# Performance work log

Hardware: AMD Instinct MI355X
Metric: run time of the kernel (lower is better)

The kernel has to match this reference:

```python
import jax, jax.numpy as jnp
import numpy as np

B, C_IN, C_OUT, N, K = 16, 128, 128, 4096, 16


def setup_inputs() -> dict:
    key = jax.random.key(0)
    k1, k2, k3, k4 = jax.random.split(key, 4)
    x = jax.random.normal(k1, (B, C_IN, N, 1), dtype=jnp.float32)
    edge_index = jax.random.randint(k2, (2, B, N, K), 0, N, dtype=jnp.int32)
    # 1x1 conv weight of BasicConv([C_IN, C_OUT], 'relu', None, bias=False)
    W = jax.random.normal(k3, (C_OUT, C_IN), dtype=jnp.float32) * (1.0 / np.sqrt(C_IN))
    # module bias param, initialized to zeros; use random here to exercise the add
    bias = jax.random.normal(k4, (1, C_OUT, 1, 1), dtype=jnp.float32) * 0.01
    return {"x": x, "edge_index": edge_index, "W": W, "bias": bias}


def reference(x, edge_index, W, bias):
    b, _, n, _ = x.shape
    # BasicConv: 1x1 conv (no bias) + ReLU
    h = jax.nn.relu(jnp.einsum('oi,binu->bonu', W, x))  # [B, C_out, N, 1]
    h2 = h[..., 0]                                       # [B, C_out, N]
    # add_self_loops: append self index along neighbor dim
    self_idx = jnp.broadcast_to(jnp.arange(n, dtype=edge_index.dtype)[None, None, :, None],
                                (2, b, n, 1))
    ei = jnp.concatenate([edge_index, self_idx], axis=-1)  # [2, B, N, K+1]
    idx = ei[0]                                            # [B, N, K+1]
    deg = ei.shape[-1]
    norm = 1.0 / deg
    # batched_index_select: gather neighbor features -> [B, C_out, N, K+1]
    x_j = jax.vmap(lambda hb, ib: hb[:, ib])(h2, idx)
    aggr = (x_j * norm).sum(axis=-1, keepdims=True)        # [B, C_out, N, 1]
    return aggr + bias
```

## Files before the change

### kernel.cpp

```cpp
#include <hip/hip_runtime.h>

#define B_    16
#define CIN_  128
#define COUT_ 128
#define N_    4096
#define K_    16

typedef __attribute__((ext_vector_type(8))) short bf16x8;
typedef __attribute__((ext_vector_type(4))) float f32x4;
typedef __attribute__((ext_vector_type(4))) int   i32x4;

__device__ inline unsigned short f2bf(float f) {
  unsigned u = __float_as_uint(f);
  u += 0x7fffu + ((u >> 16) & 1u);
  return (unsigned short)(u >> 16);
}

__global__ __launch_bounds__(256) void convW_k(
    const float* __restrict__ W, unsigned short* __restrict__ Wbf) {
  int id = blockIdx.x * 256 + threadIdx.x;
  float4 v = reinterpret_cast<const float4*>(W)[id];
  unsigned p0 = (unsigned)f2bf(v.x) | ((unsigned)f2bf(v.y) << 16);
  unsigned p1 = (unsigned)f2bf(v.z) | ((unsigned)f2bf(v.w) << 16);
  *reinterpret_cast<uint2*>(Wbf + 4 * id) = make_uint2(p0, p1);
}

__global__ __launch_bounds__(1024, 4) void gemm_relu_k(
    const unsigned short* __restrict__ Wbf, const float* __restrict__ x,
    unsigned short* __restrict__ h) {
  __shared__ unsigned short Wl[128 * 136];
  __shared__ unsigned short He[256 * 144];
  const int tid  = threadIdx.x;
  const int l    = blockIdx.x;
  const int slot = l >> 3;
  const int b    = ((l & 7) << 1) | (slot >> 4);
  const int n0   = (slot & 15) * 256;

#pragma unroll
  for (int r = 0; r < 2; ++r) {
    int id  = tid + 1024 * r;
    int co  = id >> 4;
    int seg = id & 15;
    uint4 v = reinterpret_cast<const uint4*>(Wbf)[id];
    *reinterpret_cast<uint4*>(&Wl[co * 136 + 8 * seg]) = v;
  }
  __syncthreads();

  const int lane = tid & 63;
  const int w    = tid >> 6;
  const int m    = lane & 15;
  const int quad = lane >> 4;

  const float* xb = x + (size_t)b * CIN_ * N_ + n0 + 16 * w + m;
  bf16x8 a[4];
#pragma unroll
  for (int s = 0; s < 4; ++s)
#pragma unroll
    for (int j = 0; j < 8; ++j)
      a[s][j] = (short)f2bf(xb[(size_t)(32 * s + 8 * quad + j) * N_]);

  const int nrow = 16 * w + 4 * quad;
#pragma unroll
  for (int t = 0; t < 8; ++t) {
    f32x4 c = {0.f, 0.f, 0.f, 0.f};
#pragma unroll
    for (int s = 0; s < 4; ++s) {
      bf16x8 bf = *reinterpret_cast<const bf16x8*>(
          &Wl[(16 * t + m) * 136 + 32 * s + 8 * quad]);
      c = __builtin_amdgcn_mfma_f32_16x16x32_bf16(a[s], bf, c, 0, 0, 0);
    }
    int co = 16 * t + m;
#pragma unroll
    for (int r = 0; r < 4; ++r) {
      float v = c[r] > 0.f ? c[r] : 0.f;
      He[(nrow + r) * 144 + co] = f2bf(v);
    }
  }
  __syncthreads();

  unsigned short* hb = h + ((size_t)b * N_ + n0) * COUT_;
  const int seg = tid & 15;
  const int nr  = tid >> 4;
#pragma unroll
  for (int p = 0; p < 4; ++p) {
    int n = nr + 64 * p;
    uint4 v = *reinterpret_cast<const uint4*>(&He[n * 144 + 8 * seg]);
    *reinterpret_cast<uint4*>(hb + (size_t)n * COUT_ + 8 * seg) = v;
  }
}

__global__ __launch_bounds__(256, 4) void aggr_k(
    const unsigned short* __restrict__ h, const int* __restrict__ ei,
    const float* __restrict__ bias, float* __restrict__ out) {
  __shared__ int idx_t[17 * 64];
  const int tid  = threadIdx.x;
  const int l    = blockIdx.x;
  const int rest = l >> 3;
  const int b    = ((l & 7) << 1) | (rest >> 6);
  const int n0   = (rest & 63) * 64;

  {
    int n  = tid >> 2;
    int kq = tid & 3;
    i32x4 v = __builtin_nontemporal_load(
        reinterpret_cast<const i32x4*>(ei + ((size_t)b * N_ + n0 + n) * K_) + kq);
    idx_t[(4 * kq + 0) * 64 + n] = v.x;
    idx_t[(4 * kq + 1) * 64 + n] = v.y;
    idx_t[(4 * kq + 2) * 64 + n] = v.z;
    idx_t[(4 * kq + 3) * 64 + n] = v.w;
    if (tid < 64) idx_t[16 * 64 + tid] = n0 + tid;
  }
  __syncthreads();

  const int q = tid & 15;
  const int g = tid >> 4;
  const unsigned short* hb = h + (size_t)b * N_ * COUT_;

  float acc[4][8];
#pragma unroll
  for (int j = 0; j < 4; ++j)
#pragma unroll
    for (int c = 0; c < 8; ++c) acc[j][c] = 0.f;

#pragma unroll 2
  for (int k = 0; k < 17; ++k) {
    uint4 v[4];
#pragma unroll
    for (int j = 0; j < 4; ++j) {
      int node = idx_t[k * 64 + 4 * g + j];
      v[j] = *reinterpret_cast<const uint4*>(hb + (size_t)node * COUT_ + 8 * q);
    }
#pragma unroll
    for (int j = 0; j < 4; ++j) {
      acc[j][0] += __uint_as_float(v[j].x << 16);
      acc[j][1] += __uint_as_float(v[j].x & 0xffff0000u);
      acc[j][2] += __uint_as_float(v[j].y << 16);
      acc[j][3] += __uint_as_float(v[j].y & 0xffff0000u);
      acc[j][4] += __uint_as_float(v[j].z << 16);
      acc[j][5] += __uint_as_float(v[j].z & 0xffff0000u);
      acc[j][6] += __uint_as_float(v[j].w << 16);
      acc[j][7] += __uint_as_float(v[j].w & 0xffff0000u);
    }
  }

  const float norm = 1.0f / 17.0f;
  const float4 bv0 = *reinterpret_cast<const float4*>(bias + 8 * q);
  const float4 bv1 = *reinterpret_cast<const float4*>(bias + 8 * q + 4);
  float* ob = out + (size_t)b * COUT_ * N_ + n0 + 4 * g;
#pragma unroll
  for (int c = 0; c < 8; ++c) {
    int co = 8 * q + c;
    float bb = (c < 4) ? ((c == 0) ? bv0.x : (c == 1) ? bv0.y : (c == 2) ? bv0.z : bv0.w)
                       : ((c == 4) ? bv1.x : (c == 5) ? bv1.y : (c == 6) ? bv1.z : bv1.w);
    float4 r;
    r.x = acc[0][c] * norm + bb;
    r.y = acc[1][c] * norm + bb;
    r.z = acc[2][c] * norm + bb;
    r.w = acc[3][c] * norm + bb;
    *reinterpret_cast<float4*>(ob + (size_t)co * N_) = r;
  }
}

extern "C" void kernel_launch(void* const* d_in, const int* in_sizes, int n_in,
                              void* d_out, int out_size, void* d_ws, size_t ws_size,
                              hipStream_t stream) {
  const float* x    = (const float*)d_in[0];
  const int*   ei   = (const int*)d_in[1];
  const float* W    = (const float*)d_in[2];
  const float* bias = (const float*)d_in[3];
  float* out = (float*)d_out;
  unsigned short* h   = (unsigned short*)d_ws;
  unsigned short* Wbf = (unsigned short*)((char*)d_ws + (size_t)B_ * N_ * COUT_ * 2);

  convW_k<<<dim3(16), 256, 0, stream>>>(W, Wbf);
  gemm_relu_k<<<dim3(256), 1024, 0, stream>>>(Wbf, x, h);
  aggr_k<<<dim3(B_ * N_ / 64), 256, 0, stream>>>(h, ei, bias, out);
}
```

Before: 112.7 us.

## Fuse weight conversion, GEMM and aggregation into one kernel with per-batch-group barrier

Merges the three launches into one persistent-style kernel. Each block converts W to bf16 itself and issues the x loads before the W staging. After writing its h tile it waits on a global atomic barrier shared by the 32 blocks that cover the same pair of batches, then performs the neighbor aggregation for four 64-node tiles, reusing the He shared buffer for the index tables. This removes launch gaps and the separate W conversion pass. In exchange it relies on all 32 blocks of a group being co-resident, adds a spin-wait, and converts W redundantly in every block.

```diff
diff --git a/kernel.cpp b/kernel.cpp
--- a/kernel.cpp
+++ b/kernel.cpp
@@ -16,35 +16,19 @@
   return (unsigned short)(u >> 16);
 }
 
-__global__ __launch_bounds__(256) void convW_k(
-    const float* __restrict__ W, unsigned short* __restrict__ Wbf) {
-  int id = blockIdx.x * 256 + threadIdx.x;
-  float4 v = reinterpret_cast<const float4*>(W)[id];
-  unsigned p0 = (unsigned)f2bf(v.x) | ((unsigned)f2bf(v.y) << 16);
-  unsigned p1 = (unsigned)f2bf(v.z) | ((unsigned)f2bf(v.w) << 16);
-  *reinterpret_cast<uint2*>(Wbf + 4 * id) = make_uint2(p0, p1);
-}
+__device__ int g_bar[8 * 32];
 
-__global__ __launch_bounds__(1024, 4) void gemm_relu_k(
-    const unsigned short* __restrict__ Wbf, const float* __restrict__ x,
-    unsigned short* __restrict__ h) {
+__global__ __launch_bounds__(1024, 4) void fused_k(
+    const float* __restrict__ W, const float* __restrict__ x,
+    const int* __restrict__ ei, const float* __restrict__ bias,
+    float* __restrict__ out, unsigned short* __restrict__ h) {
   __shared__ unsigned short Wl[128 * 136];
-  __shared__ unsigned short He[256 * 144];
+  __shared__ __align__(16) unsigned short He[256 * 144];
   const int tid  = threadIdx.x;
   const int l    = blockIdx.x;
   const int slot = l >> 3;
   const int b    = ((l & 7) << 1) | (slot >> 4);
   const int n0   = (slot & 15) * 256;
-
-#pragma unroll
-  for (int r = 0; r < 2; ++r) {
-    int id  = tid + 1024 * r;
-    int co  = id >> 4;
-    int seg = id & 15;
-    uint4 v = reinterpret_cast<const uint4*>(Wbf)[id];
-    *reinterpret_cast<uint4*>(&Wl[co * 136 + 8 * seg]) = v;
-  }
-  __syncthreads();
 
   const int lane = tid & 63;
   const int w    = tid >> 6;
@@ -52,12 +36,36 @@
   const int quad = lane >> 4;
 
   const float* xb = x + (size_t)b * CIN_ * N_ + n0 + 16 * w + m;
+  float xa[32];
+#pragma unroll
+  for (int s = 0; s < 4; ++s)
+#pragma unroll
+    for (int j = 0; j < 8; ++j)
+      xa[8 * s + j] = xb[(size_t)(32 * s + 8 * quad + j) * N_];
+
+#pragma unroll
+  for (int r = 0; r < 2; ++r) {
+    int id  = tid + 1024 * r;
+    int co  = id >> 4;
+    int seg = id & 15;
+    const float4* wp = reinterpret_cast<const float4*>(W + co * CIN_ + 8 * seg);
+    float4 v0 = wp[0];
+    float4 v1 = wp[1];
+    unsigned p0 = (unsigned)f2bf(v0.x) | ((unsigned)f2bf(v0.y) << 16);
+    unsigned p1 = (unsigned)f2bf(v0.z) | ((unsigned)f2bf(v0.w) << 16);
+    unsigned p2 = (unsigned)f2bf(v1.x) | ((unsigned)f2bf(v1.y) << 16);
+    unsigned p3 = (unsigned)f2bf(v1.z) | ((unsigned)f2bf(v1.w) << 16);
+    *reinterpret_cast<uint4*>(&Wl[co * 136 + 8 * seg]) =
+        make_uint4(p0, p1, p2, p3);
+  }
+  __syncthreads();
+
   bf16x8 a[4];
 #pragma unroll
   for (int s = 0; s < 4; ++s)
 #pragma unroll
     for (int j = 0; j < 8; ++j)
-      a[s][j] = (short)f2bf(xb[(size_t)(32 * s + 8 * quad + j) * N_]);
+      a[s][j] = (short)f2bf(xa[8 * s + j]);
 
   const int nrow = 16 * w + 4 * quad;
 #pragma unroll
@@ -78,43 +86,53 @@
   }
   __syncthreads();
 
-  unsigned short* hb = h + ((size_t)b * N_ + n0) * COUT_;
-  const int seg = tid & 15;
-  const int nr  = tid >> 4;
+  {
+    unsigned short* hb = h + ((size_t)b * N_ + n0) * COUT_;
+    const int seg = tid & 15;
+    const int nr  = tid >> 4;
 #pragma unroll
-  for (int p = 0; p < 4; ++p) {
-    int n = nr + 64 * p;
-    uint4 v = *reinterpret_cast<const uint4*>(&He[n * 144 + 8 * seg]);
-    *reinterpret_cast<uint4*>(hb + (size_t)n * COUT_ + 8 * seg) = v;
+    for (int p = 0; p < 4; ++p) {
+      int n = nr + 64 * p;
+      uint4 v = *reinterpret_cast<const uint4*>(&He[n * 144 + 8 * seg]);
+      *reinterpret_cast<uint4*>(hb + (size_t)n * COUT_ + 8 * seg) = v;
+    }
   }
-}
 
-__global__ __launch_bounds__(256, 4) void aggr_k(
-    const unsigned short* __restrict__ h, const int* __restrict__ ei,
-    const float* __restrict__ bias, float* __restrict__ out) {
-  __shared__ int idx_t[17 * 64];
-  const int tid  = threadIdx.x;
-  const int l    = blockIdx.x;
-  const int rest = l >> 3;
-  const int b    = ((l & 7) << 1) | (rest >> 6);
-  const int n0   = (rest & 63) * 64;
-
-  {
-    int n  = tid >> 2;
-    int kq = tid & 3;
-    i32x4 v = __builtin_nontemporal_load(
-        reinterpret_cast<const i32x4*>(ei + ((size_t)b * N_ + n0 + n) * K_) + kq);
-    idx_t[(4 * kq + 0) * 64 + n] = v.x;
-    idx_t[(4 * kq + 1) * 64 + n] = v.y;
-    idx_t[(4 * kq + 2) * 64 + n] = v.z;
-    idx_t[(4 * kq + 3) * 64 + n] = v.w;
-    if (tid < 64) idx_t[16 * 64 + tid] = n0 + tid;
+  __syncthreads();
+  if (tid == 0) {
+    int* cnt = &g_bar[(l & 7) * 32];
+    int base = __hip_atomic_fetch_add(cnt, 1, __ATOMIC_RELEASE,
+                                      __HIP_MEMORY_SCOPE_AGENT);
+    int target = (base & ~31) + 32;
+    while (__hip_atomic_load(cnt, __ATOMIC_RELAXED,
+                             __HIP_MEMORY_SCOPE_AGENT) < target)
+      __builtin_amdgcn_s_sleep(4);
   }
   __syncthreads();
 
-  const int q = tid & 15;
-  const int g = tid >> 4;
-  const unsigned short* hb = h + (size_t)b * N_ * COUT_;
+  const int s4    = tid >> 8;
+  const int t2    = tid & 255;
+  const int rest2 = (l >> 3) + 32 * s4;
+  const int b2    = ((l & 7) << 1) | (rest2 >> 6);
+  const int n02   = (rest2 & 63) * 64;
+  int* idxs = reinterpret_cast<int*>(He) + s4 * (17 * 64);
+
+  {
+    int n  = t2 >> 2;
+    int kq = t2 & 3;
+    i32x4 v = __builtin_nontemporal_load(
+        reinterpret_cast<const i32x4*>(ei + ((size_t)b2 * N_ + n02 + n) * K_) + kq);
+    idxs[(4 * kq + 0) * 64 + n] = v.x;
+    idxs[(4 * kq + 1) * 64 + n] = v.y;
+    idxs[(4 * kq + 2) * 64 + n] = v.z;
+    idxs[(4 * kq + 3) * 64 + n] = v.w;
+    if (t2 < 64) idxs[16 * 64 + t2] = n02 + t2;
+  }
+  __syncthreads();
+
+  const int q = t2 & 15;
+  const int g = t2 >> 4;
+  const unsigned short* hb2 = h + (size_t)b2 * N_ * COUT_;
 
   float acc[4][8];
 #pragma unroll
@@ -127,8 +145,8 @@
     uint4 v[4];
 #pragma unroll
     for (int j = 0; j < 4; ++j) {
-      int node = idx_t[k * 64 + 4 * g + j];
-      v[j] = *reinterpret_cast<const uint4*>(hb + (size_t)node * COUT_ + 8 * q);
+      int node = idxs[k * 64 + 4 * g + j];
+      v[j] = *reinterpret_cast<const uint4*>(hb2 + (size_t)node * COUT_ + 8 * q);
     }
 #pragma unroll
     for (int j = 0; j < 4; ++j) {
@@ -146,7 +164,7 @@
   const float norm = 1.0f / 17.0f;
   const float4 bv0 = *reinterpret_cast<const float4*>(bias + 8 * q);
   const float4 bv1 = *reinterpret_cast<const float4*>(bias + 8 * q + 4);
-  float* ob = out + (size_t)b * COUT_ * N_ + n0 + 4 * g;
+  float* ob = out + (size_t)b2 * COUT_ * N_ + n02 + 4 * g;
 #pragma unroll
   for (int c = 0; c < 8; ++c) {
     int co = 8 * q + c;
@@ -169,10 +187,7 @@
   const float* W    = (const float*)d_in[2];
   const float* bias = (const float*)d_in[3];
   float* out = (float*)d_out;
-  unsigned short* h   = (unsigned short*)d_ws;
-  unsigned short* Wbf = (unsigned short*)((char*)d_ws + (size_t)B_ * N_ * COUT_ * 2);
+  unsigned short* h = (unsigned short*)d_ws;
 
-  convW_k<<<dim3(16), 256, 0, stream>>>(W, Wbf);
-  gemm_relu_k<<<dim3(256), 1024, 0, stream>>>(Wbf, x, h);
-  aggr_k<<<dim3(B_ * N_ / 64), 256, 0, stream>>>(h, ei, bias, out);
+  fused_k<<<dim3(256), dim3(1024), 0, stream>>>(W, x, ei, bias, out, h);
 }
```

Result: slower. 120.3 us (+6.7%).
